# Kernel optimization log

Hardware: AMD Instinct MI355X
Metric: run time of the kernel (lower is better)

## Reference

```python
import jax, jax.numpy as jnp
import numpy as np

N = 4096          # number of points in the minibatch
POINT_DIM = 64    # latent/data dimensionality used to synthesize valid distance matrices


def _pairwise_dist(x):
    # x: [N, D] -> [N, N] Euclidean distance matrix
    sq = jnp.sum(x * x, axis=1)
    d2 = sq[:, None] + sq[None, :] - 2.0 * (x @ x.T)
    d = jnp.sqrt(jnp.maximum(d2, 0.0))
    return d * (1.0 - jnp.eye(x.shape[0], dtype=x.dtype))  # exact zero diagonal


def _mst_pairs(D):
    """0-dim Vietoris-Rips persistence pairs == edges of the minimum spanning tree.

    Vectorized Prim's algorithm: lax.scan over N-1 steps, O(N) per step.
    Returns int32 [N-1, 2] (parent, child) edge index pairs. Indices are
    non-differentiable (matches the .detach() in the original module).
    """
    D = jax.lax.stop_gradient(D)
    n = D.shape[0]
    INF = jnp.asarray(jnp.inf, D.dtype)
    in_tree = jnp.zeros(n, dtype=bool).at[0].set(True)
    min_dist = D[0].at[0].set(INF)          # best known edge weight from tree to each node
    parent = jnp.zeros(n, dtype=jnp.int32)  # tree endpoint realizing that edge

    def step(carry, _):
        min_dist, parent, in_tree = carry
        masked = jnp.where(in_tree, INF, min_dist)
        j = jnp.argmin(masked).astype(jnp.int32)
        pair = jnp.stack([parent[j], j])
        in_tree = in_tree.at[j].set(True)
        better = (D[j] < min_dist) & (~in_tree)
        parent = jnp.where(better, j, parent)
        min_dist = jnp.where(better, D[j], min_dist)
        return (min_dist, parent, in_tree), pair

    _, pairs = jax.lax.scan(step, (min_dist, parent, in_tree), None, length=n - 1)
    return pairs  # [N-1, 2]


def _sig_error(s1, s2):
    # ((s1 - s2) ** 2).sum() ** 0.5
    diff = s1 - s2
    return jnp.sqrt(jnp.sum(diff * diff))


def _gather(D, pairs):
    return D[pairs[:, 0], pairs[:, 1]]


def setup_inputs() -> dict:
    key = jax.random.key(0)
    k1, k2 = jax.random.split(key)
    x1 = jax.random.normal(k1, (N, POINT_DIM), dtype=jnp.float32)
    x2 = jax.random.normal(k2, (N, POINT_DIM), dtype=jnp.float32)
    return {
        "distances1": _pairwise_dist(x1),
        "distances2": _pairwise_dist(x2),
    }


def reference(distances1, distances2):
    # pairs: 0-dim persistence pairings (MST edges), computed on detached distances
    pairs1 = _mst_pairs(distances1)
    pairs2 = _mst_pairs(distances2)

    # match_edges == 'symmetric'
    sig1 = _gather(distances1, pairs1)
    sig1_2 = _gather(distances2, pairs1)
    sig2 = _gather(distances2, pairs2)
    sig2_1 = _gather(distances1, pairs2)

    distance1_2 = _sig_error(sig1, sig1_2)
    distance2_1 = _sig_error(sig2, sig2_1)
    distance = distance1_2 + distance2_1

    # metrics.matched_pairs: |set(pairs1) ∩ set(pairs2)| (MST edges are unique)
    eq = (pairs1[:, None, :] == pairs2[None, :, :]).all(-1)  # [N-1, N-1]
    matched_pairs = jnp.sum(eq.any(-1)).astype(jnp.float32)

    return distance, distance1_2, distance2_1, matched_pairs
```

## Files before the change

### kernel.cpp

```cpp
#include <hip/hip_runtime.h>
#include <math.h>

#define N 4096
#define ROUNDS 12
#define INFKEY 0xFFFFFFFFFFFFFFFFULL
#define LCAP 64
#define EC (N - 1)
#define M2 (2 * EC)
#define MBLK 32
#define RPB (N / MBLK)
#define RPW (RPB / 16)

typedef unsigned long long u64;
typedef unsigned int u32;
typedef unsigned short u16;
typedef unsigned char u8;

#define WS_PARENT(ws) ((int*)((char*)(ws) + 0))
#define WS_RCNT(ws)   ((int*)((char*)(ws) + 32768))
#define WS_RTHR(ws)   ((float*)((char*)(ws) + 65536))
#define WS_EDGES(ws)  ((int2*)((char*)(ws) + 98304))
#define WS_CAND(ws)   ((u64*)((char*)(ws) + 163840))
#define WS_META(ws)   ((int*)((char*)(ws) + 294912))
#define WS_LISTS(ws)  ((u64*)((char*)(ws) + 295168))


__device__ __forceinline__ void mat_barrier(int* cnt, int* gen, int target) {
    __syncthreads();
    if (threadIdx.x == 0) {
        __threadfence();
        int old = atomicAdd(cnt, 1);
        if (old == MBLK - 1) {
            __hip_atomic_store(cnt, 0, __ATOMIC_RELAXED, __HIP_MEMORY_SCOPE_AGENT);
            __hip_atomic_store(gen, target, __ATOMIC_RELEASE, __HIP_MEMORY_SCOPE_AGENT);
        } else {
            while (__hip_atomic_load(gen, __ATOMIC_ACQUIRE, __HIP_MEMORY_SCOPE_AGENT) < target)
                __builtin_amdgcn_s_sleep(1);
        }
        __threadfence();
    }
    __syncthreads();
}

__global__ __launch_bounds__(512) void build_kernel(const float* __restrict__ D1,
                                                    const float* __restrict__ D2,
                                                    int* __restrict__ rowcount,
                                                    float* __restrict__ rthresh,
                                                    u64* __restrict__ lists,
                                                    u64* __restrict__ cand,
                                                    int* __restrict__ meta) {
    const int gb = blockIdx.x;
    const int tid = threadIdx.x;

    if (gb < 4) {
        int i = 2 * N + (gb * 512 + tid) * 4;
        cand[i] = INFKEY; cand[i + 1] = INFKEY; cand[i + 2] = INFKEY; cand[i + 3] = INFKEY;
    } else if (gb == 4 && tid < 64) {
        meta[tid] = 0;
    }

    const int m = gb >> 9;
    const int wid = tid >> 6, lane = tid & 63;
    const int row = (gb & 511) * 8 + wid;
    const float* __restrict__ Drow = (m ? D2 : D1) + (size_t)row * N;
    const float INF = __builtin_inff();

    float4 v[16];
#pragma unroll
    for (int it = 0; it < 16; ++it)
        v[it] = *(const float4*)(Drow + it * 256 + lane * 4);

    u64 kmin = INFKEY;
    float sm = 0.f;
#pragma unroll
    for (int it = 0; it < 16; ++it) {
        float e4[4] = {v[it].x, v[it].y, v[it].z, v[it].w};
#pragma unroll
        for (int s = 0; s < 4; ++s) {
            float x = e4[s];
            if (x > 0.f) {
                u64 k = ((u64)__float_as_uint(x) << 12) | (unsigned)(it * 256 + lane * 4 + s);
                if (k < kmin) kmin = k;
            }
            sm += x;
        }
    }
#pragma unroll
    for (int off = 32; off > 0; off >>= 1) {
        u64 o = __shfl_xor(kmin, off, 64);
        if (o < kmin) kmin = o;
        sm += __shfl_xor(sm, off, 64);
    }
    const float mn = __uint_as_float((u32)(kmin >> 12));
    const float mean = sm * (1.f / 4095.f);
    float T = mn + 0.25f * (mean - mn);

    int mycnt, total;
    for (int iter = 0; iter < 10; ++iter) {
        mycnt = 0;
#pragma unroll
        for (int it = 0; it < 16; ++it) {
            mycnt += (v[it].x > 0.f && v[it].x < T);
            mycnt += (v[it].y > 0.f && v[it].y < T);
            mycnt += (v[it].z > 0.f && v[it].z < T);
            mycnt += (v[it].w > 0.f && v[it].w < T);
        }
        total = mycnt;
#pragma unroll
        for (int off = 32; off > 0; off >>= 1) total += __shfl_xor(total, off, 64);
        if (total <= LCAP) break;
        T = mn + 0.5f * (T - mn);
    }

    int incl = mycnt;
#pragma unroll
    for (int d = 1; d < 64; d <<= 1) {
        int o = __shfl_up(incl, d, 64);
        if (lane >= d) incl += o;
    }
    int pos = incl - mycnt;

    u64* lp = lists + ((size_t)m * N + row) * LCAP;
#pragma unroll
    for (int it = 0; it < 16; ++it) {
        float e4[4] = {v[it].x, v[it].y, v[it].z, v[it].w};
#pragma unroll
        for (int s = 0; s < 4; ++s) {
            float x = e4[s];
            if (x > 0.f && x < T) {
                if (pos < LCAP)
                    lp[pos] = ((u64)__float_as_uint(x) << 12) | (unsigned)(it * 256 + lane * 4 + s);
                ++pos;
            }
        }
    }
    if (lane == 0) {
        rowcount[m * N + row] = total;
        rthresh[m * N + row] = T;
        cand[m * N + row] = ((kmin >> 12) << 24) | ((u64)row << 12) | (kmin & 0xFFF);
    }
}

__global__ __launch_bounds__(1024) void solve_kernel(const float* __restrict__ D1,
                                                     const float* __restrict__ D2,
                                                     const int* __restrict__ rcnt,
                                                     const float* __restrict__ rthr,
                                                     const u64* __restrict__ lists,
                                                     u64* __restrict__ cand_g,
                                                     int2* __restrict__ edges_g,
                                                     int* __restrict__ parent_g,
                                                     int* __restrict__ meta,
                                                     float* __restrict__ out) {
    const int b = blockIdx.x;
    const int m = b / MBLK;
    const int bm = b - m * MBLK;
    const int tid = threadIdx.x;
    const int wid = tid >> 6, lane = tid & 63;
    const float* __restrict__ D = m ? D2 : D1;
    const int* __restrict__ grc = rcnt + m * N;
    const float* __restrict__ gth = rthr + m * N;
    const u64* __restrict__ gls = lists + (size_t)m * N * LCAP;
    int2* __restrict__ ged = edges_g + (size_t)m * N;
    int* __restrict__ gpar = parent_g + m * N;
    int* bcnt = meta + m * 16 + 1;
    int* bgen = meta + m * 16 + 2;
    int* garr = meta + 40;
    const float INF = __builtin_inff();

    __shared__ __align__(16) char SM[57344];
    int* scomp = (int*)SM;
    u64* scand = (u64*)(SM + 16384);
    u16* sresc = (u16*)(SM + 49152);
    __shared__ u8 sexh[RPB];
    __shared__ int snres, secnt, scnt, swar[16];

    for (int i = tid; i < N; i += 1024) scomp[i] = i;
    for (int i = tid; i < RPB; i += 1024) sexh[i] = 0;
    if (tid == 0) secnt = 0;
    int phase = 0;
    bool done = false;

    for (int round = 0; round < ROUNDS && !done; ++round) {
        const int buf = round & 1;
        u64* __restrict__ gcand = cand_g + (size_t)buf * 2 * N + m * N;

        if (round > 0) {
            u64* __restrict__ gcand_o = cand_g + (size_t)(buf ^ 1) * 2 * N + m * N;
            for (int i = tid; i < N; i += 1024) scand[i] = INFKEY;
            if (tid == 0) snres = 0;
            __syncthreads();

            {
                const int lbase = wid * RPW;
                int cnts[RPW];
                u64 ent[RPW];
#pragma unroll
                for (int r = 0; r < RPW; ++r) {
                    int lrow = lbase + r;
                    cnts[r] = sexh[lrow] ? -1 : grc[bm * RPB + lrow];
                }
#pragma unroll
                for (int r = 0; r < RPW; ++r) {
                    int lrow = lbase + r;
                    ent[r] = (cnts[r] > lane) ? gls[(size_t)(bm * RPB + lrow) * LCAP + lane]
                                              : INFKEY;
                }
#pragma unroll
                for (int r = 0; r < RPW; ++r) {
                    const int lrow = lbase + r;
                    const int row = bm * RPB + lrow;
                    if (cnts[r] < 0) {
                        if (lane == 0) { int i = atomicAdd(&snres, 1); sresc[i] = (u16)(row | 0x1000); }
                        continue;
                    }
                    if (cnts[r] > LCAP) {
                        if (lane == 0) { int i = atomicAdd(&snres, 1); sresc[i] = (u16)(row | 0x4000); }
                        continue;
                    }
                    const int c = scomp[row];
                    u64 e = ent[r];
                    u64 best = (e != INFKEY && scomp[(int)(e & 0xFFF)] != c) ? e : INFKEY;
#pragma unroll
                    for (int off = 32; off > 0; off >>= 1) {
                        u64 o = __shfl_xor(best, off, 64);
                        if (o < best) best = o;
                    }
                    if (lane == 0) {
                        if (best != INFKEY) {
                            u64 key = ((best >> 12) << 24) | ((u64)row << 12) | (best & 0xFFF);
                            if (key < scand[c]) atomicMin(&scand[c], key);
                        } else {
                            sexh[lrow] = 1;
                            int i = atomicAdd(&snres, 1); sresc[i] = (u16)(row | 0x1000);
                        }
                    }
                }
            }
            __syncthreads();
            for (int c = tid; c < N; c += 1024) {
                u64 v = scand[c];
                if (v != INFKEY) atomicMin(&gcand[c], v);
            }
            mat_barrier(bcnt, bgen, ++phase);

            if (tid < RPB)
                __hip_atomic_store(&gcand_o[bm * RPB + tid], INFKEY,
                                   __ATOMIC_RELAXED, __HIP_MEMORY_SCOPE_AGENT);
            for (int i = tid; i < snres; i += 1024) {
                u16 e = sresc[i];
                if (e & 0x1000) {
                    int row = e & 0xFFF;
                    int c = scomp[row];
                    u64 cc = gcand[c];
                    float w = (cc == INFKEY) ? INF : __uint_as_float((u32)(cc >> 24));
                    if (!(gth[row] < w)) sresc[i] = 0xFFFF;
                }
            }
            __syncthreads();
            {
                const int nres = snres;
                for (int i = wid; i < nres; i += 16) {
                    u16 e = sresc[i];
                    if (e == 0xFFFF) continue;
                    int row = (int)(e & 0xFFF);
                    int c = scomp[row];
                    const float* Drow = D + (size_t)row * N;
                    u64 best = INFKEY;
                    for (int j0 = lane * 4; j0 < N; j0 += 256) {
                        float4 d = *(const float4*)(Drow + j0);
                        int4 cj = *(const int4*)(scomp + j0);
                        if (cj.x != c) { u64 k = ((u64)__float_as_uint(d.x) << 12) | (unsigned)(j0 + 0); if (k < best) best = k; }
                        if (cj.y != c) { u64 k = ((u64)__float_as_uint(d.y) << 12) | (unsigned)(j0 + 1); if (k < best) best = k; }
                        if (cj.z != c) { u64 k = ((u64)__float_as_uint(d.z) << 12) | (unsigned)(j0 + 2); if (k < best) best = k; }
                        if (cj.w != c) { u64 k = ((u64)__float_as_uint(d.w) << 12) | (unsigned)(j0 + 3); if (k < best) best = k; }
                    }
#pragma unroll
                    for (int off = 32; off > 0; off >>= 1) {
                        u64 o = __shfl_xor(best, off, 64);
                        if (o < best) best = o;
                    }
                    if (lane == 0 && best != INFKEY) {
                        u64 key = ((best >> 12) << 24) | ((u64)row << 12) | (best & 0xFFF);
                        atomicMin(&gcand[c], key);
                    }
                }
            }
            mat_barrier(bcnt, bgen, ++phase);
        }

        for (int i = tid; i < N; i += 1024) scand[i] = gcand[i];
        __syncthreads();
        u16* slink = sresc;
        for (int c = tid; c < N; c += 1024) {
            int l = scomp[c];
            if (l == c) {
                u64 k = scand[c];
                if (k != INFKEY) {
                    int v = (int)(k & 0xFFF);
                    int u = (int)((k >> 12) & 0xFFF);
                    int t = scomp[v];
                    u64 tk = scand[t];
                    int mutual = 0;
                    if (tk != INFKEY) {
                        int tv = (int)(tk & 0xFFF);
                        mutual = (scomp[tv] == c);
                    }
                    if (mutual) {
                        if (c < t) {
                            if (bm == 0) { int idx = atomicAdd(&secnt, 1); ged[idx] = make_int2(u, v); }
                        } else l = t;
                    } else {
                        if (bm == 0) { int idx = atomicAdd(&secnt, 1); ged[idx] = make_int2(u, v); }
                        l = t;
                    }
                }
            }
            slink[c] = (u16)l;
        }
        __syncthreads();
        for (int c = tid; c < N; c += 1024) scomp[c] = slink[c];
        __syncthreads();
        for (int c = tid; c < N; c += 1024) {
            int r = scomp[c];
            int n = scomp[r];
            while (n != r) { r = n; n = scomp[r]; }
            scomp[c] = r;
        }
        __syncthreads();
        if (tid == 0) scnt = 0;
        __syncthreads();
        int local = 0;
        for (int c = tid; c < N; c += 1024) local += (scomp[c] == c) ? 1 : 0;
        atomicAdd(&scnt, local);
        __syncthreads();
        done = (scnt == 1);
        __syncthreads();
    }

    if (bm == 0) {
        u32* uvp  = (u32*)SM;
        u16* off  = (u16*)(SM + 16384);
        u16* adj  = (u16*)(SM + 24576);
        u16* succ = (u16*)(SM + 40960);
        u16* rnk  = (u16*)(SM + 16384);
        u32* minp = (u32*)(SM + 40960);

        __syncthreads();
        const int ec = secnt;
        for (int i = tid; i < ec; i += 1024) {
            int2 e = ged[i];
            uvp[i] = ((u32)e.x << 16) | (u32)e.y;
        }
        for (int i = tid; i < 2048; i += 1024) ((u32*)off)[i] = 0;
        __syncthreads();
        for (int i = tid; i < ec; i += 1024) {
            u32 w = uvp[i];
            int u = (int)(w >> 16), v = (int)(w & 0xFFFF);
            atomicAdd((u32*)off + (u >> 1), 1u << ((u & 1) * 16));
            atomicAdd((u32*)off + (v >> 1), 1u << ((v & 1) * 16));
        }
        __syncthreads();
        {
            const int i0 = tid * 4;
            int d0 = off[i0], d1 = off[i0 + 1], d2 = off[i0 + 2], d3 = off[i0 + 3];
            int t0 = d0, t01 = d0 + d1, t012 = t01 + d2, tot = t012 + d3;
            int inc = tot;
#pragma unroll
            for (int d = 1; d < 64; d <<= 1) {
                int o = __shfl_up(inc, d, 64);
                if (lane >= d) inc += o;
            }
            if (lane == 63) swar[wid] = inc;
            __syncthreads();
            if (wid == 0) {
                int v = (lane < 16) ? swar[lane] : 0;
                int vin = v;
#pragma unroll
                for (int d = 1; d < 16; d <<= 1) {
                    int o = __shfl_up(v, d, 64);
                    if (lane >= d) v += o;
                }
                if (lane < 16) swar[lane] = v - vin;
            }
            __syncthreads();
            int base = swar[wid] + (inc - tot);
            off[i0] = (u16)base;
            off[i0 + 1] = (u16)(base + t0);
            off[i0 + 2] = (u16)(base + t01);
            off[i0 + 3] = (u16)(base + t012);
        }
        __syncthreads();
        for (int e = tid; e < M2; e += 1024) {
            int i = e >> 1;
            u32 w = uvp[i];
            int src = (e & 1) ? (int)(w & 0xFFFF) : (int)(w >> 16);
            u32 old = atomicAdd((u32*)off + (src >> 1), 1u << ((src & 1) * 16));
            u32 slot = (old >> ((src & 1) * 16)) & 0xFFFFu;
            adj[slot] = (u16)e;
            succ[e] = (u16)slot;
        }
        __syncthreads();
        const int e0 = adj[0];
        {
            u16 nsv[8];
            int k = 0;
            for (int e = tid; e < M2; e += 1024) {
                int i = e >> 1;
                u32 w = uvp[i];
                int v = (e & 1) ? (int)(w >> 16) : (int)(w & 0xFFFF);
                int st = succ[e ^ 1];
                int start = (v == 0) ? 0 : off[v - 1];
                int end = off[v];
                int ns = (st + 1 < end) ? st + 1 : start;
                nsv[k++] = adj[ns];
            }
            __syncthreads();
            k = 0;
            for (int e = tid; e < M2; e += 1024) succ[e] = nsv[k++];
        }
        __syncthreads();
        for (int e = tid; e < M2; e += 1024) {
            u16 s = succ[e];
            if (s == (u16)e0) { succ[e] = (u16)e; rnk[e] = 0; }
            else rnk[e] = 1;
        }
        __syncthreads();
        for (int it = 0; it < 13; ++it) {
            u16 nr[8], s2[8];
            int k = 0;
            for (int e = tid; e < M2; e += 1024) {
                u16 s1 = succ[e];
                u16 r1 = rnk[e];
                nr[k] = (u16)(r1 + rnk[s1]);
                s2[k] = succ[s1];
                ++k;
            }
            __syncthreads();
            k = 0;
            for (int e = tid; e < M2; e += 1024) { rnk[e] = nr[k]; succ[e] = s2[k]; ++k; }
            __syncthreads();
        }
        for (int i = tid; i < N; i += 1024) minp[i] = 0xFFFFFFFFu;
        __syncthreads();
        for (int e = tid; e < M2; e += 1024) {
            int i = e >> 1;
            u32 w = uvp[i];
            int dst = (e & 1) ? (int)(w >> 16) : (int)(w & 0xFFFF);
            int srcv = (e & 1) ? (int)(w & 0xFFFF) : (int)(w >> 16);
            u32 p = (u32)(M2 - 1) - (u32)rnk[e];
            atomicMin(&minp[dst], (p << 16) | (u32)srcv);
        }
        __syncthreads();
        for (int v = tid; v < N; v += 1024) gpar[v] = (v == 0) ? 0 : (int)(minp[v] & 0xFFFFu);
    }

    __syncthreads();
    if (tid == 0) {
        __threadfence();
        atomicAdd(garr, 1);
    }
    if (b != 0) return;
    if (tid == 0) {
        while (__hip_atomic_load(garr, __ATOMIC_ACQUIRE, __HIP_MEMORY_SCOPE_AGENT) < 2 * MBLK)
            __builtin_amdgcn_s_sleep(1);
        __threadfence();
    }
    __syncthreads();

    {
        float* rs12 = (float*)SM;
        float* rs21 = (float*)(SM + 64);
        int* rm = (int*)(SM + 128);
        const int* p1 = parent_g;
        const int* p2 = parent_g + N;
        float s12 = 0.f, s21 = 0.f;
        int mcnt = 0;
        for (int c = 1 + tid; c < N; c += 1024) {
            int a = p1[c];
            int bb = p2[c];
            float e1 = D1[(size_t)a * N + c] - D2[(size_t)a * N + c];
            float e2 = D2[(size_t)bb * N + c] - D1[(size_t)bb * N + c];
            s12 += e1 * e1;
            s21 += e2 * e2;
            mcnt += (a == bb) ? 1 : 0;
        }
#pragma unroll
        for (int off = 32; off > 0; off >>= 1) {
            s12 += __shfl_xor(s12, off, 64);
            s21 += __shfl_xor(s21, off, 64);
            mcnt += __shfl_xor(mcnt, off, 64);
        }
        if (lane == 0) { rs12[wid] = s12; rs21[wid] = s21; rm[wid] = mcnt; }
        __syncthreads();
        if (tid == 0) {
            float a = 0.f, bb = 0.f;
            int mm = 0;
#pragma unroll
            for (int w = 0; w < 16; ++w) { a += rs12[w]; bb += rs21[w]; mm += rm[w]; }
            float d12 = sqrtf(a);
            float d21 = sqrtf(bb);
            out[0] = d12 + d21;
            out[1] = d12;
            out[2] = d21;
            out[3] = (float)mm;
        }
    }
}

extern "C" void kernel_launch(void* const* d_in, const int* in_sizes, int n_in,
                              void* d_out, int out_size, void* d_ws, size_t ws_size,
                              hipStream_t stream) {
    const float* D1 = (const float*)d_in[0];
    const float* D2 = (const float*)d_in[1];

    int* parent = WS_PARENT(d_ws);
    int* rcnt = WS_RCNT(d_ws);
    float* rthr = WS_RTHR(d_ws);
    int2* edges = WS_EDGES(d_ws);
    u64* cand = WS_CAND(d_ws);
    int* meta = WS_META(d_ws);
    u64* lists = WS_LISTS(d_ws);

    build_kernel<<<1024, 512, 0, stream>>>(D1, D2, rcnt, rthr, lists, cand, meta);
    solve_kernel<<<2 * MBLK, 1024, 0, stream>>>(D1, D2, rcnt, rthr, lists, cand,
                                                edges, parent, meta, (float*)d_out);
}
```

Baseline: 302.0 us.

## Fold per-row candidate list build into the persistent solve kernel

Removes the 1024-block build kernel and moves its per-row min/threshold/list construction into the 64-block solve kernel, followed by a grid barrier. A tiny init kernel now only clears candidate buffers and meta counters. This cuts one heavy launch, but the 128MB distance scan now runs on just 64 blocks and re-reads each row from memory for every threshold iteration instead of keeping it in registers.

```diff
diff --git a/kernel.cpp b/kernel.cpp
--- a/kernel.cpp
+++ b/kernel.cpp
@@ -42,110 +42,20 @@
     __syncthreads();
 }
 
-__global__ __launch_bounds__(512) void build_kernel(const float* __restrict__ D1,
-                                                    const float* __restrict__ D2,
-                                                    int* __restrict__ rowcount,
-                                                    float* __restrict__ rthresh,
-                                                    u64* __restrict__ lists,
-                                                    u64* __restrict__ cand,
+__global__ __launch_bounds__(1024) void init_kernel(u64* __restrict__ cand,
                                                     int* __restrict__ meta) {
-    const int gb = blockIdx.x;
     const int tid = threadIdx.x;
-
-    if (gb < 4) {
-        int i = 2 * N + (gb * 512 + tid) * 4;
-        cand[i] = INFKEY; cand[i + 1] = INFKEY; cand[i + 2] = INFKEY; cand[i + 3] = INFKEY;
-    } else if (gb == 4 && tid < 64) {
-        meta[tid] = 0;
-    }
-
-    const int m = gb >> 9;
-    const int wid = tid >> 6, lane = tid & 63;
-    const int row = (gb & 511) * 8 + wid;
-    const float* __restrict__ Drow = (m ? D2 : D1) + (size_t)row * N;
-    const float INF = __builtin_inff();
-
-    float4 v[16];
-#pragma unroll
-    for (int it = 0; it < 16; ++it)
-        v[it] = *(const float4*)(Drow + it * 256 + lane * 4);
-
-    u64 kmin = INFKEY;
-    float sm = 0.f;
-#pragma unroll
-    for (int it = 0; it < 16; ++it) {
-        float e4[4] = {v[it].x, v[it].y, v[it].z, v[it].w};
-#pragma unroll
-        for (int s = 0; s < 4; ++s) {
-            float x = e4[s];
-            if (x > 0.f) {
-                u64 k = ((u64)__float_as_uint(x) << 12) | (unsigned)(it * 256 + lane * 4 + s);
-                if (k < kmin) kmin = k;
-            }
-            sm += x;
-        }
-    }
-#pragma unroll
-    for (int off = 32; off > 0; off >>= 1) {
-        u64 o = __shfl_xor(kmin, off, 64);
-        if (o < kmin) kmin = o;
-        sm += __shfl_xor(sm, off, 64);
-    }
-    const float mn = __uint_as_float((u32)(kmin >> 12));
-    const float mean = sm * (1.f / 4095.f);
-    float T = mn + 0.25f * (mean - mn);
-
-    int mycnt, total;
-    for (int iter = 0; iter < 10; ++iter) {
-        mycnt = 0;
-#pragma unroll
-        for (int it = 0; it < 16; ++it) {
-            mycnt += (v[it].x > 0.f && v[it].x < T);
-            mycnt += (v[it].y > 0.f && v[it].y < T);
-            mycnt += (v[it].z > 0.f && v[it].z < T);
-            mycnt += (v[it].w > 0.f && v[it].w < T);
-        }
-        total = mycnt;
-#pragma unroll
-        for (int off = 32; off > 0; off >>= 1) total += __shfl_xor(total, off, 64);
-        if (total <= LCAP) break;
-        T = mn + 0.5f * (T - mn);
-    }
-
-    int incl = mycnt;
-#pragma unroll
-    for (int d = 1; d < 64; d <<= 1) {
-        int o = __shfl_up(incl, d, 64);
-        if (lane >= d) incl += o;
-    }
-    int pos = incl - mycnt;
-
-    u64* lp = lists + ((size_t)m * N + row) * LCAP;
-#pragma unroll
-    for (int it = 0; it < 16; ++it) {
-        float e4[4] = {v[it].x, v[it].y, v[it].z, v[it].w};
-#pragma unroll
-        for (int s = 0; s < 4; ++s) {
-            float x = e4[s];
-            if (x > 0.f && x < T) {
-                if (pos < LCAP)
-                    lp[pos] = ((u64)__float_as_uint(x) << 12) | (unsigned)(it * 256 + lane * 4 + s);
-                ++pos;
-            }
-        }
-    }
-    if (lane == 0) {
-        rowcount[m * N + row] = total;
-        rthresh[m * N + row] = T;
-        cand[m * N + row] = ((kmin >> 12) << 24) | ((u64)row << 12) | (kmin & 0xFFF);
-    }
+#pragma unroll
+    for (int j = 0; j < 8; ++j)
+        cand[2 * N + tid * 8 + j] = INFKEY;
+    if (tid < 64) meta[tid] = 0;
 }
 
 __global__ __launch_bounds__(1024) void solve_kernel(const float* __restrict__ D1,
                                                      const float* __restrict__ D2,
-                                                     const int* __restrict__ rcnt,
-                                                     const float* __restrict__ rthr,
-                                                     const u64* __restrict__ lists,
+                                                     int* __restrict__ rcnt,
+                                                     float* __restrict__ rthr,
+                                                     u64* __restrict__ lists,
                                                      u64* __restrict__ cand_g,
                                                      int2* __restrict__ edges_g,
                                                      int* __restrict__ parent_g,
@@ -157,9 +67,9 @@
     const int tid = threadIdx.x;
     const int wid = tid >> 6, lane = tid & 63;
     const float* __restrict__ D = m ? D2 : D1;
-    const int* __restrict__ grc = rcnt + m * N;
-    const float* __restrict__ gth = rthr + m * N;
-    const u64* __restrict__ gls = lists + (size_t)m * N * LCAP;
+    int* __restrict__ grc = rcnt + m * N;
+    float* __restrict__ gth = rthr + m * N;
+    u64* __restrict__ gls = lists + (size_t)m * N * LCAP;
     int2* __restrict__ ged = edges_g + (size_t)m * N;
     int* __restrict__ gpar = parent_g + m * N;
     int* bcnt = meta + m * 16 + 1;
@@ -179,6 +89,103 @@
     if (tid == 0) secnt = 0;
     int phase = 0;
     bool done = false;
+
+    for (int r8 = 0; r8 < RPW; ++r8) {
+        const int lrow = wid * RPW + r8;
+        const int row = bm * RPB + lrow;
+        const float* __restrict__ Drow = D + (size_t)row * N;
+
+        u64 kmin = INFKEY;
+        float sm = 0.f;
+        for (int it4 = 0; it4 < 4; ++it4) {
+            float4 vv[4];
+#pragma unroll
+            for (int j = 0; j < 4; ++j)
+                vv[j] = *(const float4*)(Drow + (it4 * 4 + j) * 256 + lane * 4);
+#pragma unroll
+            for (int j = 0; j < 4; ++j) {
+                const int base = (it4 * 4 + j) * 256 + lane * 4;
+                float e4[4] = {vv[j].x, vv[j].y, vv[j].z, vv[j].w};
+#pragma unroll
+                for (int s = 0; s < 4; ++s) {
+                    float x = e4[s];
+                    if (x > 0.f) {
+                        u64 k = ((u64)__float_as_uint(x) << 12) | (unsigned)(base + s);
+                        if (k < kmin) kmin = k;
+                    }
+                    sm += x;
+                }
+            }
+        }
+#pragma unroll
+        for (int off = 32; off > 0; off >>= 1) {
+            u64 o = __shfl_xor(kmin, off, 64);
+            if (o < kmin) kmin = o;
+            sm += __shfl_xor(sm, off, 64);
+        }
+        const float mn = __uint_as_float((u32)(kmin >> 12));
+        const float mean = sm * (1.f / 4095.f);
+        float T = mn + 0.25f * (mean - mn);
+
+        int mycnt = 0, total = 0;
+        for (int iter = 0; iter < 10; ++iter) {
+            mycnt = 0;
+            for (int it4 = 0; it4 < 4; ++it4) {
+                float4 vv[4];
+#pragma unroll
+                for (int j = 0; j < 4; ++j)
+                    vv[j] = *(const float4*)(Drow + (it4 * 4 + j) * 256 + lane * 4);
+#pragma unroll
+                for (int j = 0; j < 4; ++j) {
+                    mycnt += (vv[j].x > 0.f && vv[j].x < T);
+                    mycnt += (vv[j].y > 0.f && vv[j].y < T);
+                    mycnt += (vv[j].z > 0.f && vv[j].z < T);
+                    mycnt += (vv[j].w > 0.f && vv[j].w < T);
+                }
+            }
+            total = mycnt;
+#pragma unroll
+            for (int off = 32; off > 0; off >>= 1) total += __shfl_xor(total, off, 64);
+            if (total <= LCAP) break;
+            T = mn + 0.5f * (T - mn);
+        }
+
+        int incl = mycnt;
+#pragma unroll
+        for (int d = 1; d < 64; d <<= 1) {
+            int o = __shfl_up(incl, d, 64);
+            if (lane >= d) incl += o;
+        }
+        int pos = incl - mycnt;
+
+        u64* lp = gls + (size_t)row * LCAP;
+        for (int it4 = 0; it4 < 4; ++it4) {
+            float4 vv[4];
+#pragma unroll
+            for (int j = 0; j < 4; ++j)
+                vv[j] = *(const float4*)(Drow + (it4 * 4 + j) * 256 + lane * 4);
+#pragma unroll
+            for (int j = 0; j < 4; ++j) {
+                const int base = (it4 * 4 + j) * 256 + lane * 4;
+                float e4[4] = {vv[j].x, vv[j].y, vv[j].z, vv[j].w};
+#pragma unroll
+                for (int s = 0; s < 4; ++s) {
+                    float x = e4[s];
+                    if (x > 0.f && x < T) {
+                        if (pos < LCAP)
+                            lp[pos] = ((u64)__float_as_uint(x) << 12) | (unsigned)(base + s);
+                        ++pos;
+                    }
+                }
+            }
+        }
+        if (lane == 0) {
+            grc[row] = total;
+            gth[row] = T;
+            cand_g[(size_t)m * N + row] = ((kmin >> 12) << 24) | ((u64)row << 12) | (kmin & 0xFFF);
+        }
+    }
+    mat_barrier(bcnt, bgen, ++phase);
 
     for (int round = 0; round < ROUNDS && !done; ++round) {
         const int buf = round & 1;
@@ -521,7 +528,7 @@
     int* meta = WS_META(d_ws);
     u64* lists = WS_LISTS(d_ws);
 
-    build_kernel<<<1024, 512, 0, stream>>>(D1, D2, rcnt, rthr, lists, cand, meta);
+    init_kernel<<<1, 1024, 0, stream>>>(cand, meta);
     solve_kernel<<<2 * MBLK, 1024, 0, stream>>>(D1, D2, rcnt, rthr, lists, cand,
                                                 edges, parent, meta, (float*)d_out);
 }
```

Result: slower. 427.2 us (+41.5%).
